# Optimization experiments

Hardware: AMD Instinct MI355X
Metric: run time of the kernel (lower is better)

## Reference

```python
import jax, jax.numpy as jnp
from jax import lax
import numpy as np

B, L, F = 4, 1024, 32
DM, NL, DS, DC, EX, NH = 256, 4, 16, 4, 2, 4
DI = EX * DM            # 512 inner channels
DTR = (DM + 15) // 16   # dt_rank = 16


def setup_inputs() -> dict:
    key = jax.random.key(0)
    ks = jax.random.split(key, 12)
    s = 0.02
    rn = lambda k, shape: jax.random.normal(k, shape, jnp.float32) * s
    return dict(
        x=jax.random.normal(ks[0], (B, L, F), jnp.float32),
        proj_w=rn(ks[1], (DM, F)), proj_b=jnp.zeros((DM,), jnp.float32),
        inproj_w=rn(ks[2], (NL, 2 * DI, DM)),
        conv_w=rn(ks[3], (NL, DI, DC)), conv_b=jnp.zeros((NL, DI), jnp.float32),
        xproj_w=rn(ks[4], (NL, DTR + 2 * DS, DI)),
        dtproj_w=rn(ks[5], (NL, DI, DTR)), dtproj_b=rn(ks[6], (NL, DI)),
        A_log=jnp.tile(jnp.log(jnp.arange(1, DS + 1, dtype=jnp.float32))[None, None, :], (NL, DI, 1)),
        Dp=jnp.ones((NL, DI), jnp.float32),
        outproj_w=rn(ks[7], (NL, DM, DI)),
        ln_g=jnp.ones((NL, DM), jnp.float32), ln_b=jnp.zeros((NL, DM), jnp.float32),
        head_w1=rn(ks[8], (DM, DM)), head_b1=jnp.zeros((DM,), jnp.float32),
        head_w2=rn(ks[9], (NH, DM)), head_b2=jnp.zeros((NH,), jnp.float32),
    )


def _layernorm(x, g, b, eps=1e-5):
    mu = x.mean(axis=-1, keepdims=True)
    var = ((x - mu) ** 2).mean(axis=-1, keepdims=True)
    return (x - mu) * lax.rsqrt(var + eps) * g + b


def _mamba(x, inw, cw, cb, xpw, dtw, dtb, A_log, Dp, outw):
    b, l, _ = x.shape
    xz = x @ inw.T                       # (b,l,2*DI)
    u, z = xz[..., :DI], xz[..., DI:]
    # causal depthwise conv1d, kernel DC
    up = jnp.pad(u, ((0, 0), (DC - 1, 0), (0, 0)))
    uc = sum(up[:, k:k + l, :] * cw[:, k] for k in range(DC)) + cb
    uc = jax.nn.silu(uc)
    dbc = uc @ xpw.T                     # (b,l,DTR+2*DS)
    dt, Bc, Cc = dbc[..., :DTR], dbc[..., DTR:DTR + DS], dbc[..., DTR + DS:]
    delta = jax.nn.softplus(dt @ dtw.T + dtb)   # (b,l,DI)
    A = -jnp.exp(A_log)                  # (DI,DS)

    def step(h, inp):
        d_t, B_t, C_t, u_t = inp         # (b,DI),(b,DS),(b,DS),(b,DI)
        h = jnp.exp(d_t[..., None] * A) * h + (d_t * u_t)[..., None] * B_t[:, None, :]
        return h, jnp.einsum('bdn,bn->bd', h, C_t)

    h0 = jnp.zeros((b, DI, DS), x.dtype)
    xs = tuple(jnp.swapaxes(a, 0, 1) for a in (delta, Bc, Cc, uc))
    _, ys = lax.scan(step, h0, xs)       # ys: (l,b,DI)
    y = jnp.swapaxes(ys, 0, 1) + uc * Dp
    return (y * jax.nn.silu(z)) @ outw.T


def reference(x, proj_w, proj_b, inproj_w, conv_w, conv_b, xproj_w, dtproj_w, dtproj_b,
              A_log, Dp, outproj_w, ln_g, ln_b, head_w1, head_b1, head_w2, head_b2):
    h = x @ proj_w.T + proj_b
    for i in range(NL):
        blk = _mamba(h, inproj_w[i], conv_w[i], conv_b[i], xproj_w[i],
                     dtproj_w[i], dtproj_b[i], A_log[i], Dp[i], outproj_w[i])
        h = h + _layernorm(blk, ln_g[i], ln_b[i])
    p = h.mean(axis=1)                   # (b,DM) pool over time
    hid = jax.nn.relu(p @ head_w1.T + head_b1)
    return hid @ head_w2.T + head_b2     # (b,NH)
```

## Files before the change

kernel.cpp:

```cpp
#include <hip/hip_runtime.h>
#include <hip/hip_fp16.h>
#include <math.h>

#define LTOT 1024
#define BB   4
#define F_IN 32
#define DM   256
#define DI   512
#define DS   16
#define DTRN 16
#define NXP  48
#define NLAY 4
#define NH   4
#define NC   16
#define CLEN 64
#define ROWS (BB*LTOT)

typedef _Float16 half8 __attribute__((ext_vector_type(8)));
typedef float f32x16 __attribute__((ext_vector_type(16)));

__device__ __forceinline__ float siluf_(float x) { return x / (1.0f + expf(-x)); }
__device__ __forceinline__ float softplusf_(float x) {
    if (x > 20.f) return x;
    if (x < -20.f) return expf(x);
    return log1pf(expf(x));
}

__device__ __forceinline__ void split16(float x, unsigned short& hi, unsigned short& lo) {
    __half h = __float2half(x);
    hi = *(unsigned short*)&h;
    float r = x - __half2float(h);
    __half l = __float2half(r);
    lo = *(unsigned short*)&l;
}

__device__ __forceinline__ size_t fragAddr(int r, int k, int Kd) {
    return ((size_t)((r >> 5) * (Kd >> 4) + (k >> 4)) << 9)
         + (size_t)(((((k >> 3) & 1) << 5) + (r & 31)) * 8 + (k & 7));
}

__global__ __launch_bounds__(256) void k_init(const float* __restrict__ x,
                                              const float* __restrict__ pw,
                                              const float* __restrict__ pb,
                                              const float* __restrict__ inw,
                                              const float* __restrict__ outw,
                                              float* __restrict__ h,
                                              unsigned short* __restrict__ hh,
                                              unsigned short* __restrict__ hl,
                                              unsigned short* __restrict__ iwh,
                                              unsigned short* __restrict__ iwl,
                                              unsigned short* __restrict__ owh,
                                              unsigned short* __restrict__ owl) {
    __shared__ float wl[DM][33];
    __shared__ float xl[16][32];
    int bid = blockIdx.x, t = threadIdx.x;
    if (bid < 1536) {
        int q = bid * 256 + t;
        ushort4 h4, l4;
        if (q < 262144) {
            float4 v = ((const float4*)inw)[q];
            split16(v.x, h4.x, l4.x); split16(v.y, h4.y, l4.y);
            split16(v.z, h4.z, l4.z); split16(v.w, h4.w, l4.w);
            int row = q >> 6, k0 = (q & 63) * 4;
            int lay = row >> 10, rIn = row & 1023;
            size_t fa = (size_t)lay * 262144 + fragAddr(rIn, k0, 256);
            *(ushort4*)(iwh + fa) = h4;
            *(ushort4*)(iwl + fa) = l4;
        } else {
            int rq = q - 262144;
            float4 v = ((const float4*)outw)[rq];
            split16(v.x, h4.x, l4.x); split16(v.y, h4.y, l4.y);
            split16(v.z, h4.z, l4.z); split16(v.w, h4.w, l4.w);
            int row = rq >> 7, k0 = (rq & 127) * 4;
            int lay = row >> 8, rIn = row & 255;
            size_t fa = (size_t)lay * 131072 + fragAddr(rIn, k0, 512);
            *(ushort4*)(owh + fa) = h4;
            *(ushort4*)(owl + fa) = l4;
        }
        return;
    }
    int r0 = (bid - 1536) * 16;
    for (int i = t; i < DM * 32 / 4; i += 256) {
        float4 v = ((const float4*)pw)[i];
        int c = i / 8, k = (i % 8) * 4;
        wl[c][k] = v.x; wl[c][k + 1] = v.y; wl[c][k + 2] = v.z; wl[c][k + 3] = v.w;
    }
    for (int i = t; i < 16 * 32 / 4; i += 256) {
        float4 v = ((const float4*)(x + (size_t)r0 * F_IN))[i];
        int r = i / 8, k = (i % 8) * 4;
        xl[r][k] = v.x; xl[r][k + 1] = v.y; xl[r][k + 2] = v.z; xl[r][k + 3] = v.w;
    }
    __syncthreads();
    int c = t;
    float bias = pb[c];
    float acc[16];
#pragma unroll
    for (int r = 0; r < 16; ++r) acc[r] = bias;
    for (int k = 0; k < 32; ++k) {
        float w = wl[c][k];
#pragma unroll
        for (int r = 0; r < 16; ++r) acc[r] = fmaf(xl[r][k], w, acc[r]);
    }
#pragma unroll
    for (int r = 0; r < 16; ++r) {
        int rr = r0 + r;
        h[(size_t)rr * DM + c] = acc[r];
        unsigned short vh, vl; split16(acc[r], vh, vl);
        size_t fa = fragAddr(rr, c, 256);
        hh[fa] = vh; hl[fa] = vl;
    }
}

__global__ __launch_bounds__(256) void k_gemm_xz(const unsigned short* __restrict__ Ahp,
                                                 const unsigned short* __restrict__ Alp,
                                                 const unsigned short* __restrict__ Bhp,
                                                 const unsigned short* __restrict__ Blp,
                                                 float* __restrict__ C) {
    int t = threadIdx.x;
    int bx = blockIdx.x & 7;
    int by = blockIdx.x >> 3;
    int lane = t & 63, wid = t >> 6;
    int fr = lane & 31, fg = lane >> 5;
    int wr = wid >> 1, wc = wid & 1;
    int rt = by * 2 + wr;
    int ct0 = bx * 4 + wc * 2;
    const half8* pAh = (const half8*)Ahp + (size_t)rt * 1024 + lane;
    const half8* pAl = (const half8*)Alp + (size_t)rt * 1024 + lane;
    const half8* pB0h = (const half8*)Bhp + (size_t)ct0 * 1024 + lane;
    const half8* pB0l = (const half8*)Blp + (size_t)ct0 * 1024 + lane;
    const half8* pB1h = pB0h + 1024;
    const half8* pB1l = pB0l + 1024;
    f32x16 acc[2] = {};
    half8 ah = pAh[0], al = pAl[0];
    half8 b0h = pB0h[0], b0l = pB0l[0], b1h = pB1h[0], b1l = pB1l[0];
#pragma unroll
    for (int kt = 0; kt < 16; ++kt) {
        half8 nah, nal, nb0h, nb0l, nb1h, nb1l;
        if (kt < 15) {
            int o = (kt + 1) * 64;
            nah = pAh[o]; nal = pAl[o];
            nb0h = pB0h[o]; nb0l = pB0l[o];
            nb1h = pB1h[o]; nb1l = pB1l[o];
        }
        acc[0] = __builtin_amdgcn_mfma_f32_32x32x16_f16(ah, b0h, acc[0], 0, 0, 0);
        acc[0] = __builtin_amdgcn_mfma_f32_32x32x16_f16(ah, b0l, acc[0], 0, 0, 0);
        acc[0] = __builtin_amdgcn_mfma_f32_32x32x16_f16(al, b0h, acc[0], 0, 0, 0);
        acc[1] = __builtin_amdgcn_mfma_f32_32x32x16_f16(ah, b1h, acc[1], 0, 0, 0);
        acc[1] = __builtin_amdgcn_mfma_f32_32x32x16_f16(ah, b1l, acc[1], 0, 0, 0);
        acc[1] = __builtin_amdgcn_mfma_f32_32x32x16_f16(al, b1h, acc[1], 0, 0, 0);
        if (kt < 15) { ah = nah; al = nal; b0h = nb0h; b0l = nb0l; b1h = nb1h; b1l = nb1l; }
    }
    float* Cp = C + (size_t)(by * 64 + wr * 32) * 1024 + bx * 128 + wc * 64;
#pragma unroll
    for (int fc = 0; fc < 2; ++fc) {
#pragma unroll
        for (int reg = 0; reg < 16; ++reg) {
            int row = (reg & 3) + 8 * (reg >> 2) + 4 * fg;
            Cp[(size_t)row * 1024 + fc * 32 + fr] = acc[fc][reg];
        }
    }
}

__global__ __launch_bounds__(256) void k_dbcp(const float* __restrict__ xz,
                                              const float* __restrict__ cw,
                                              const float* __restrict__ cb,
                                              const float* __restrict__ xpw,
                                              float* __restrict__ uc,
                                              float* __restrict__ dbp) {
    __shared__ float us[32][132];
    __shared__ float wsd[48][132];
    int t = threadIdx.x;
    int kp = blockIdx.x & 3;
    int r0 = (blockIdx.x >> 2) * 32;
    int k0 = kp * 128;
    float4* us4 = (float4*)us;
    float4* ws4 = (float4*)wsd;
#pragma unroll
    for (int j = 0; j < 4; ++j) {
        int i = t + j * 256;
        int r = i >> 5, kq = i & 31;
        int rr = r0 + r, d = k0 + kq * 4;
        int tt = rr & (LTOT - 1);
        float4 acc = make_float4(cb[d], cb[d + 1], cb[d + 2], cb[d + 3]);
#pragma unroll
        for (int k = 0; k < 4; ++k) {
            int ts = tt - 3 + k;
            if (ts < 0) continue;
            float4 u = *(const float4*)(xz + (size_t)(rr - 3 + k) * 1024 + d);
            acc.x = fmaf(u.x, cw[(d + 0) * 4 + k], acc.x);
            acc.y = fmaf(u.y, cw[(d + 1) * 4 + k], acc.y);
            acc.z = fmaf(u.z, cw[(d + 2) * 4 + k], acc.z);
            acc.w = fmaf(u.w, cw[(d + 3) * 4 + k], acc.w);
        }
        acc.x = siluf_(acc.x); acc.y = siluf_(acc.y); acc.z = siluf_(acc.z); acc.w = siluf_(acc.w);
        us4[r * 33 + kq] = acc;
        *(float4*)(uc + (size_t)rr * DI + d) = acc;
    }
#pragma unroll
    for (int j = 0; j < 6; ++j) {
        int i = t + j * 256;
        int r = i >> 5, kq = i & 31;
        ws4[r * 33 + kq] = *(const float4*)(xpw + (size_t)r * DI + k0 + kq * 4);
    }
    __syncthreads();
    int tx = t & 15, ty = t >> 4;
    const float4* ua = us4 + (ty * 2) * 33;
    const float4* ub = ua + 33;
    const float4* w0p = ws4 + (tx * 3) * 33;
    const float4* w1p = w0p + 33;
    const float4* w2p = w0p + 66;
    float acc[2][3] = {};
#pragma unroll 4
    for (int kq = 0; kq < 32; ++kq) {
        float4 u0 = ua[kq], u1 = ub[kq];
        float4 w0 = w0p[kq], w1 = w1p[kq], w2 = w2p[kq];
        acc[0][0] = fmaf(u0.x, w0.x, acc[0][0]); acc[0][0] = fmaf(u0.y, w0.y, acc[0][0]);
        acc[0][0] = fmaf(u0.z, w0.z, acc[0][0]); acc[0][0] = fmaf(u0.w, w0.w, acc[0][0]);
        acc[0][1] = fmaf(u0.x, w1.x, acc[0][1]); acc[0][1] = fmaf(u0.y, w1.y, acc[0][1]);
        acc[0][1] = fmaf(u0.z, w1.z, acc[0][1]); acc[0][1] = fmaf(u0.w, w1.w, acc[0][1]);
        acc[0][2] = fmaf(u0.x, w2.x, acc[0][2]); acc[0][2] = fmaf(u0.y, w2.y, acc[0][2]);
        acc[0][2] = fmaf(u0.z, w2.z, acc[0][2]); acc[0][2] = fmaf(u0.w, w2.w, acc[0][2]);
        acc[1][0] = fmaf(u1.x, w0.x, acc[1][0]); acc[1][0] = fmaf(u1.y, w0.y, acc[1][0]);
        acc[1][0] = fmaf(u1.z, w0.z, acc[1][0]); acc[1][0] = fmaf(u1.w, w0.w, acc[1][0]);
        acc[1][1] = fmaf(u1.x, w1.x, acc[1][1]); acc[1][1] = fmaf(u1.y, w1.y, acc[1][1]);
        acc[1][1] = fmaf(u1.z, w1.z, acc[1][1]); acc[1][1] = fmaf(u1.w, w1.w, acc[1][1]);
        acc[1][2] = fmaf(u1.x, w2.x, acc[1][2]); acc[1][2] = fmaf(u1.y, w2.y, acc[1][2]);
        acc[1][2] = fmaf(u1.z, w2.z, acc[1][2]); acc[1][2] = fmaf(u1.w, w2.w, acc[1][2]);
    }
    float* outp = dbp + (size_t)(r0 + ty * 2) * 192 + kp * 48 + tx * 3;
    outp[0] = acc[0][0]; outp[1] = acc[0][1]; outp[2] = acc[0][2];
    outp[192] = acc[1][0]; outp[193] = acc[1][1]; outp[194] = acc[1][2];
}

__global__ __launch_bounds__(256) void k_dbcr(const float* __restrict__ dbp,
                                              const float* __restrict__ dtw,
                                              const float* __restrict__ dtb,
                                              float* __restrict__ delta,
                                              float* __restrict__ BC) {
    __shared__ float dbl[16][NXP];
    int t = threadIdx.x;
    int r0 = blockIdx.x * 16;
    {
        int r = t >> 4, c3 = (t & 15) * 3;
        const float* pp = dbp + (size_t)(r0 + r) * 192 + c3;
#pragma unroll
        for (int j = 0; j < 3; ++j) {
            float s = pp[j] + pp[48 + j] + pp[96 + j] + pp[144 + j];
            dbl[r][c3 + j] = s;
            int cj = c3 + j;
            if (cj >= 16) BC[(size_t)(r0 + r) * 32 + (cj - 16)] = s;
        }
    }
    __syncthreads();
    {
        int c0 = t * 2;
        float wd0[16], wd1[16];
        const float4* q0 = (const float4*)(dtw + (size_t)c0 * 16);
        const float4* q1 = (const float4*)(dtw + (size_t)(c0 + 1) * 16);
#pragma unroll
        for (int j = 0; j < 4; ++j) { *(float4*)&wd0[j * 4] = q0[j]; *(float4*)&wd1[j * 4] = q1[j]; }
        float bb0 = dtb[c0], bb1 = dtb[c0 + 1];
        for (int r = 0; r < 16; ++r) {
            float s0 = bb0, s1 = bb1;
#pragma unroll
            for (int k = 0; k < 16; ++k) {
                float dv = dbl[r][k];
                s0 = fmaf(dv, wd0[k], s0);
                s1 = fmaf(dv, wd1[k], s1);
            }
            *(float2*)(delta + (size_t)(r0 + r) * DI + c0) =
                make_float2(softplusf_(s0), softplusf_(s1));
        }
    }
}

__global__ __launch_bounds__(256) void k_scanA(const float* __restrict__ delta,
                                               const float* __restrict__ uc,
                                               const float* __restrict__ BC,
                                               const float* __restrict__ A_log,
                                               float* __restrict__ P,
                                               float* __restrict__ hL) {
    __shared__ float2 du2[CLEN][16];
    __shared__ float  Bl[CLEN][16];
    int bid = blockIdx.x;
    int c = bid & 15, dblk = (bid >> 4) & 31, b = bid >> 9;
    int d0 = dblk * 16, t0 = c * CLEN;
    int t = threadIdx.x;
    {
        int row = t >> 2, hf = (t & 3) * 4;
        size_t rbase = (size_t)(b * LTOT + t0 + row);
        float4 dv = *(const float4*)(delta + rbase * DI + d0 + hf);
        float4 uv = *(const float4*)(uc + rbase * DI + d0 + hf);
        float4* dst = (float4*)&du2[row][hf];
        dst[0] = make_float4(dv.x, uv.x, dv.y, uv.y);
        dst[1] = make_float4(dv.z, uv.z, dv.w, uv.w);
        *(float4*)&Bl[row][hf] = *(const float4*)(BC + rbase * 32 + hf);
    }
    __syncthreads();
    int n = t & 15, dn = t >> 4;
    float Ac = -expf(A_log[(size_t)(d0 + dn) * DS + n]);
    float h = 0.f, Pp = 1.f;
#pragma unroll 8
    for (int k = 0; k < CLEN; ++k) {
        float2 du = du2[k][dn];
        float Bv = Bl[k][n];
        float a = expf(du.x * Ac);
        Pp *= a;
        h = fmaf(a, h, du.x * du.y * Bv);
    }
    size_t idx = ((size_t)(b * NC + c)) * (DI * DS) + (size_t)d0 * DS + t;
    P[idx] = Pp;
    hL[idx] = h;
}

__global__ __launch_bounds__(256) void k_scanC(const float* __restrict__ delta,
                                               const float* __restrict__ uc,
                                               const float* __restrict__ BC,
                                               const float* __restrict__ A_log,
                                               const float* __restrict__ P,
                                               const float* __restrict__ hL,
                                               const float* __restrict__ Dp,
                                               const float* __restrict__ xz,
                                               unsigned short* __restrict__ yh,
                                               unsigned short* __restrict__ yl) {
    __shared__ float2 du2[CLEN][16];
    __shared__ float2 bc2[CLEN][16];
    __shared__ float  ytmp[16][16][20];
    int bid = blockIdx.x;
    int c = bid & 15, dblk = (bid >> 4) & 31, b = bid >> 9;
    int d0 = dblk * 16, t0 = c * CLEN;
    int t = threadIdx.x;
    {
        int row = t >> 2, hf = (t & 3) * 4;
        size_t rbase = (size_t)(b * LTOT + t0 + row);
        float4 dv = *(const float4*)(delta + rbase * DI + d0 + hf);
        float4 uv = *(const float4*)(uc + rbase * DI + d0 + hf);
        float4* dst = (float4*)&du2[row][hf];
        dst[0] = make_float4(dv.x, uv.x, dv.y, uv.y);
        dst[1] = make_float4(dv.z, uv.z, dv.w, uv.w);
        float4 bv = *(const float4*)(BC + rbase * 32 + hf);
        float4 cv = *(const float4*)(BC + rbase * 32 + 16 + hf);
        float4* bdst = (float4*)&bc2[row][hf];
        bdst[0] = make_float4(bv.x, cv.x, bv.y, cv.y);
        bdst[1] = make_float4(bv.z, cv.z, bv.w, cv.w);
    }
    __syncthreads();
    int n = t & 15, dn = t >> 4;
    float Ac = -expf(A_log[(size_t)(d0 + dn) * DS + n]);
    float Hin = 0.f;
    for (int cc = 0; cc < c; ++cc) {
        size_t idx = ((size_t)(b * NC + cc)) * (DI * DS) + (size_t)d0 * DS + t;
        Hin = fmaf(P[idx], Hin, hL[idx]);
    }
    float h = Hin;
    int rdn = t & 15, rk = t >> 4;
    float DpV = Dp[d0 + rdn];
    for (int s = 0; s < CLEN / 16; ++s) {
#pragma unroll
        for (int kk = 0; kk < 16; ++kk) {
            int k = s * 16 + kk;
            float2 du = du2[k][dn];
            float2 bc = bc2[k][n];
            float a = expf(du.x * Ac);
            h = fmaf(a, h, du.x * du.y * bc.x);
            ytmp[kk][dn][n] = h * bc.y;
        }
        __syncthreads();
        {
            const float* rowp = &ytmp[rk][rdn][0];
            float4 v0 = *(const float4*)(rowp + 0);
            float4 v1 = *(const float4*)(rowp + 4);
            float4 v2 = *(const float4*)(rowp + 8);
            float4 v3 = *(const float4*)(rowp + 12);
            float y = ((v0.x + v0.y) + (v0.z + v0.w)) + ((v1.x + v1.y) + (v1.z + v1.w))
                    + ((v2.x + v2.y) + (v2.z + v2.w)) + ((v3.x + v3.y) + (v3.z + v3.w));
            float uu = du2[s * 16 + rk][rdn].y;
            size_t rb2 = (size_t)(b * LTOT + t0 + s * 16 + rk);
            float z = xz[rb2 * 1024 + 512 + d0 + rdn];
            float val = fmaf(uu, DpV, y) * siluf_(z);
            unsigned short vh, vl; split16(val, vh, vl);
            size_t fa = fragAddr((int)rb2, d0 + rdn, 512);
            yh[fa] = vh; yl[fa] = vl;
        }
        __syncthreads();
    }
}

__global__ __launch_bounds__(256) void k_gemm_out(const unsigned short* __restrict__ Ahp,
                                                  const unsigned short* __restrict__ Alp,
                                                  const unsigned short* __restrict__ Bhp,
                                                  const unsigned short* __restrict__ Blp,
                                                  float* __restrict__ p01,
                                                  float* __restrict__ p23) {
    int t = threadIdx.x;
    int bx = blockIdx.x & 1;
    int by = (blockIdx.x >> 1) & 63;
    int kp = blockIdx.x >> 7;
    int lane = t & 63, wid = t >> 6;
    int fr = lane & 31, fg = lane >> 5;
    int wr = wid >> 1, wc = wid & 1;
    int rt = by * 2 + wr;
    int ct0 = bx * 4 + wc * 2;
    const half8* pAh = (const half8*)Ahp + (size_t)rt * 2048 + (size_t)kp * 512 + lane;
    const half8* pAl = (const half8*)Alp + (size_t)rt * 2048 + (size_t)kp * 512 + lane;
    const half8* pB0h = (const half8*)Bhp + (size_t)ct0 * 2048 + (size_t)kp * 512 + lane;
    const half8* pB0l = (const half8*)Blp + (size_t)ct0 * 2048 + (size_t)kp * 512 + lane;
    const half8* pB1h = pB0h + 2048;
    const half8* pB1l = pB0l + 2048;
    f32x16 acc[2] = {};
    half8 ah = pAh[0], al = pAl[0];
    half8 b0h = pB0h[0], b0l = pB0l[0], b1h = pB1h[0], b1l = pB1l[0];
#pragma unroll
    for (int kt = 0; kt < 8; ++kt) {
        half8 nah, nal, nb0h, nb0l, nb1h, nb1l;
        if (kt < 7) {
            int o = (kt + 1) * 64;
            nah = pAh[o]; nal = pAl[o];
            nb0h = pB0h[o]; nb0l = pB0l[o];
            nb1h = pB1h[o]; nb1l = pB1l[o];
        }
        acc[0] = __builtin_amdgcn_mfma_f32_32x32x16_f16(ah, b0h, acc[0], 0, 0, 0);
        acc[0] = __builtin_amdgcn_mfma_f32_32x32x16_f16(ah, b0l, acc[0], 0, 0, 0);
        acc[0] = __builtin_amdgcn_mfma_f32_32x32x16_f16(al, b0h, acc[0], 0, 0, 0);
        acc[1] = __builtin_amdgcn_mfma_f32_32x32x16_f16(ah, b1h, acc[1], 0, 0, 0);
        acc[1] = __builtin_amdgcn_mfma_f32_32x32x16_f16(ah, b1l, acc[1], 0, 0, 0);
        acc[1] = __builtin_amdgcn_mfma_f32_32x32x16_f16(al, b1h, acc[1], 0, 0, 0);
        if (kt < 7) { ah = nah; al = nal; b0h = nb0h; b0l = nb0l; b1h = nb1h; b1l = nb1l; }
    }
    float* pbase = (kp < 2 ? p01 : p23) + (size_t)(kp & 1) * (ROWS * DM);
    float* Cp = pbase + (size_t)(by * 64 + wr * 32) * DM + bx * 128 + wc * 64;
#pragma unroll
    for (int fc = 0; fc < 2; ++fc) {
#pragma unroll
        for (int reg = 0; reg < 16; ++reg) {
            int row = (reg & 3) + 8 * (reg >> 2) + 4 * fg;
            Cp[(size_t)row * DM + fc * 32 + fr] = acc[fc][reg];
        }
    }
}

__global__ __launch_bounds__(256) void k_ln_res(const float* __restrict__ p01,
                                                const float* __restrict__ p23,
                                                const float* __restrict__ g,
                                                const float* __restrict__ bb,
                                                float* __restrict__ h,
                                                unsigned short* __restrict__ hh,
                                                unsigned short* __restrict__ hl) {
    __shared__ float scratch[4];
    int r = blockIdx.x, t = threadIdx.x;
    size_t idx = (size_t)r * DM + t;
    float v = p01[idx] + p01[idx + (size_t)ROWS * DM] + p23[idx] + p23[idx + (size_t)ROWS * DM];
    float s = v;
#pragma unroll
    for (int m = 32; m >= 1; m >>= 1) s += __shfl_xor(s, m, 64);
    if ((t & 63) == 0) scratch[t >> 6] = s;
    __syncthreads();
    float mu = (scratch[0] + scratch[1] + scratch[2] + scratch[3]) * (1.f / DM);
    __syncthreads();
    float d = v - mu;
    float s2 = d * d;
#pragma unroll
    for (int m = 32; m >= 1; m >>= 1) s2 += __shfl_xor(s2, m, 64);
    if ((t & 63) == 0) scratch[t >> 6] = s2;
    __syncthreads();
    float var = (scratch[0] + scratch[1] + scratch[2] + scratch[3]) * (1.f / DM);
    float rstd = 1.f / sqrtf(var + 1e-5f);
    float nv = h[idx] + d * rstd * g[t] + bb[t];
    h[idx] = nv;
    unsigned short vh, vl; split16(nv, vh, vl);
    size_t fa = fragAddr(r, t, 256);
    hh[fa] = vh; hl[fa] = vl;
}

__global__ __launch_bounds__(256) void k_meanp(const float* __restrict__ h,
                                               float* __restrict__ part) {
    int bid = blockIdx.x;
    int b = bid >> 3, g = bid & 7;
    int t = threadIdx.x;
    float s = 0.f;
    for (int k = 0; k < 128; ++k)
        s += h[(size_t)(b * LTOT + g * 128 + k) * DM + t];
    part[(size_t)bid * DM + t] = s;
}

__global__ __launch_bounds__(256) void k_head(const float* __restrict__ part,
                                              const float* __restrict__ w1,
                                              const float* __restrict__ b1,
                                              const float* __restrict__ w2,
                                              const float* __restrict__ b2,
                                              float* __restrict__ out) {
    __shared__ float pl[DM], hl[DM];
    int b = blockIdx.x, t = threadIdx.x;
    float s = 0.f;
    for (int g = 0; g < 8; ++g) s += part[(size_t)(b * 8 + g) * DM + t];
    pl[t] = s * (1.f / LTOT);
    __syncthreads();
    float a = b1[t];
    for (int k = 0; k < DM; ++k) a = fmaf(pl[k], w1[(size_t)t * DM + k], a);
    hl[t] = fmaxf(a, 0.f);
    __syncthreads();
    if (t < NH) {
        float o = b2[t];
        for (int k = 0; k < DM; ++k) o = fmaf(hl[k], w2[(size_t)t * DM + k], o);
        out[b * NH + t] = o;
    }
}

extern "C" void kernel_launch(void* const* d_in, const int* in_sizes, int n_in,
                              void* d_out, int out_size, void* d_ws, size_t ws_size,
                              hipStream_t stream) {
    const float* x        = (const float*)d_in[0];
    const float* proj_w   = (const float*)d_in[1];
    const float* proj_b   = (const float*)d_in[2];
    const float* inproj_w = (const float*)d_in[3];
    const float* conv_w   = (const float*)d_in[4];
    const float* conv_b   = (const float*)d_in[5];
    const float* xproj_w  = (const float*)d_in[6];
    const float* dtproj_w = (const float*)d_in[7];
    const float* dtproj_b = (const float*)d_in[8];
    const float* A_log    = (const float*)d_in[9];
    const float* Dp       = (const float*)d_in[10];
    const float* outproj_w= (const float*)d_in[11];
    const float* ln_g     = (const float*)d_in[12];
    const float* ln_b     = (const float*)d_in[13];
    const float* head_w1  = (const float*)d_in[14];
    const float* head_b1  = (const float*)d_in[15];
    const float* head_w2  = (const float*)d_in[16];
    const float* head_b2  = (const float*)d_in[17];

    float* ws    = (float*)d_ws;
    float* h     = ws;
    float* xz    = h + 1048576;
    float* uc    = xz + 4194304;
    float* dbp   = uc + 2097152;
    float* delta = dbp + 786432;
    float* BC    = delta + 2097152;
    float* Pbuf  = BC + 131072;
    float* hLbuf = Pbuf + 524288;
    float* p01   = hLbuf + 524288;
    float* p23   = p01 + 2097152;
    float* part  = p23 + 2097152;
    unsigned short* h_hi  = (unsigned short*)(part + 8192);
    unsigned short* h_lo  = h_hi + 1048576;
    unsigned short* y_hi  = h_lo + 1048576;
    unsigned short* y_lo  = y_hi + 2097152;
    unsigned short* iw_hi = y_lo + 2097152;
    unsigned short* iw_lo = iw_hi + 1048576;
    unsigned short* ow_hi = iw_lo + 1048576;
    unsigned short* ow_lo = ow_hi + 524288;

    k_init<<<1792, 256, 0, stream>>>(x, proj_w, proj_b, inproj_w, outproj_w,
                                     h, h_hi, h_lo, iw_hi, iw_lo, ow_hi, ow_lo);

    for (int i = 0; i < NLAY; ++i) {
        const float* cwi  = conv_w + (size_t)i * DI * 4;
        const float* cbi  = conv_b + (size_t)i * DI;
        const float* xpw  = xproj_w + (size_t)i * NXP * DI;
        const float* dtw  = dtproj_w + (size_t)i * DI * DTRN;
        const float* dtb  = dtproj_b + (size_t)i * DI;
        const float* Ali  = A_log + (size_t)i * DI * DS;
        const float* Dpi  = Dp + (size_t)i * DI;
        const float* gi   = ln_g + (size_t)i * DM;
        const float* bi   = ln_b + (size_t)i * DM;

        k_gemm_xz<<<512, 256, 0, stream>>>(h_hi, h_lo,
                                           iw_hi + (size_t)i * 262144, iw_lo + (size_t)i * 262144, xz);
        k_dbcp<<<512, 256, 0, stream>>>(xz, cwi, cbi, xpw, uc, dbp);
        k_dbcr<<<ROWS / 16, 256, 0, stream>>>(dbp, dtw, dtb, delta, BC);
        k_scanA<<<BB * 32 * NC, 256, 0, stream>>>(delta, uc, BC, Ali, Pbuf, hLbuf);
        k_scanC<<<BB * 32 * NC, 256, 0, stream>>>(delta, uc, BC, Ali, Pbuf, hLbuf, Dpi, xz, y_hi, y_lo);
        k_gemm_out<<<512, 256, 0, stream>>>(y_hi, y_lo,
                                            ow_hi + (size_t)i * 131072, ow_lo + (size_t)i * 131072,
                                            p01, p23);
        k_ln_res<<<ROWS, 256, 0, stream>>>(p01, p23, gi, bi, h, h_hi, h_lo);
    }

    k_meanp<<<32, 256, 0, stream>>>(h, part);
    k_head<<<BB, 256, 0, stream>>>(part, head_w1, head_b1, head_w2, head_b2, (float*)d_out);
}
```

Measured before the change: 484.4 us.

## Fuse x_proj partial and reduce kernels; batch layernorm rows per block

Merges the split-K x_proj kernel and its reduction/dt_proj kernel into one kernel. Each block now covers 16 rows and loops over all four K chunks, keeping the partial sums in registers, so the dbp intermediate buffer and one launch per layer go away. Separately, the layernorm-residual kernel now processes 8 rows per block instead of one, which reuses the gamma/beta loads across rows. The cost is fewer blocks (256 and 512) with more serial work and extra barriers per block, which lowers parallelism.

```diff
diff --git a/kernel.cpp b/kernel.cpp
--- a/kernel.cpp
+++ b/kernel.cpp
@@ -161,95 +161,86 @@
     }
 }
 
-__global__ __launch_bounds__(256) void k_dbcp(const float* __restrict__ xz,
-                                              const float* __restrict__ cw,
-                                              const float* __restrict__ cb,
-                                              const float* __restrict__ xpw,
-                                              float* __restrict__ uc,
-                                              float* __restrict__ dbp) {
-    __shared__ float us[32][132];
-    __shared__ float wsd[48][132];
-    int t = threadIdx.x;
-    int kp = blockIdx.x & 3;
-    int r0 = (blockIdx.x >> 2) * 32;
-    int k0 = kp * 128;
-    float4* us4 = (float4*)us;
-    float4* ws4 = (float4*)wsd;
-#pragma unroll
-    for (int j = 0; j < 4; ++j) {
-        int i = t + j * 256;
-        int r = i >> 5, kq = i & 31;
-        int rr = r0 + r, d = k0 + kq * 4;
-        int tt = rr & (LTOT - 1);
-        float4 acc = make_float4(cb[d], cb[d + 1], cb[d + 2], cb[d + 3]);
-#pragma unroll
-        for (int k = 0; k < 4; ++k) {
-            int ts = tt - 3 + k;
-            if (ts < 0) continue;
-            float4 u = *(const float4*)(xz + (size_t)(rr - 3 + k) * 1024 + d);
-            acc.x = fmaf(u.x, cw[(d + 0) * 4 + k], acc.x);
-            acc.y = fmaf(u.y, cw[(d + 1) * 4 + k], acc.y);
-            acc.z = fmaf(u.z, cw[(d + 2) * 4 + k], acc.z);
-            acc.w = fmaf(u.w, cw[(d + 3) * 4 + k], acc.w);
-        }
-        acc.x = siluf_(acc.x); acc.y = siluf_(acc.y); acc.z = siluf_(acc.z); acc.w = siluf_(acc.w);
-        us4[r * 33 + kq] = acc;
-        *(float4*)(uc + (size_t)rr * DI + d) = acc;
-    }
-#pragma unroll
-    for (int j = 0; j < 6; ++j) {
-        int i = t + j * 256;
-        int r = i >> 5, kq = i & 31;
-        ws4[r * 33 + kq] = *(const float4*)(xpw + (size_t)r * DI + k0 + kq * 4);
-    }
-    __syncthreads();
-    int tx = t & 15, ty = t >> 4;
-    const float4* ua = us4 + (ty * 2) * 33;
-    const float4* ub = ua + 33;
-    const float4* w0p = ws4 + (tx * 3) * 33;
-    const float4* w1p = w0p + 33;
-    const float4* w2p = w0p + 66;
-    float acc[2][3] = {};
+__global__ __launch_bounds__(256) void k_dbc(const float* __restrict__ xz,
+                                             const float* __restrict__ cw,
+                                             const float* __restrict__ cb,
+                                             const float* __restrict__ xpw,
+                                             const float* __restrict__ dtw,
+                                             const float* __restrict__ dtb,
+                                             float* __restrict__ uc,
+                                             float* __restrict__ delta,
+                                             float* __restrict__ BC) {
+    __shared__ float4 us4[16 * 33];
+    __shared__ float4 ws4[48 * 33];
+    __shared__ float  dbl[16][NXP];
+    int t = threadIdx.x;
+    int r0 = blockIdx.x * 16;
+    int row = t >> 4, tx = t & 15;
+    float ps0[4], ps1[4], ps2[4];
+#pragma unroll
+    for (int kp = 0; kp < 4; ++kp) {
+        int k0 = kp * 128;
+#pragma unroll
+        for (int j = 0; j < 2; ++j) {
+            int i = t + j * 256;
+            int r = i >> 5, kq = i & 31;
+            int rr = r0 + r, d = k0 + kq * 4;
+            int tt = rr & (LTOT - 1);
+            float4 acc = make_float4(cb[d], cb[d + 1], cb[d + 2], cb[d + 3]);
+#pragma unroll
+            for (int k = 0; k < 4; ++k) {
+                int ts = tt - 3 + k;
+                if (ts < 0) continue;
+                float4 u = *(const float4*)(xz + (size_t)(rr - 3 + k) * 1024 + d);
+                acc.x = fmaf(u.x, cw[(d + 0) * 4 + k], acc.x);
+                acc.y = fmaf(u.y, cw[(d + 1) * 4 + k], acc.y);
+                acc.z = fmaf(u.z, cw[(d + 2) * 4 + k], acc.z);
+                acc.w = fmaf(u.w, cw[(d + 3) * 4 + k], acc.w);
+            }
+            acc.x = siluf_(acc.x); acc.y = siluf_(acc.y);
+            acc.z = siluf_(acc.z); acc.w = siluf_(acc.w);
+            us4[r * 33 + kq] = acc;
+            *(float4*)(uc + (size_t)rr * DI + d) = acc;
+        }
+#pragma unroll
+        for (int j = 0; j < 6; ++j) {
+            int i = t + j * 256;
+            int r = i >> 5, kq = i & 31;
+            ws4[r * 33 + kq] = *(const float4*)(xpw + (size_t)r * DI + k0 + kq * 4);
+        }
+        __syncthreads();
+        {
+            const float4* ua = us4 + row * 33;
+            const float4* w0p = ws4 + (tx * 3) * 33;
+            const float4* w1p = w0p + 33;
+            const float4* w2p = w0p + 66;
+            float a0 = 0.f, a1 = 0.f, a2 = 0.f;
 #pragma unroll 4
-    for (int kq = 0; kq < 32; ++kq) {
-        float4 u0 = ua[kq], u1 = ub[kq];
-        float4 w0 = w0p[kq], w1 = w1p[kq], w2 = w2p[kq];
-        acc[0][0] = fmaf(u0.x, w0.x, acc[0][0]); acc[0][0] = fmaf(u0.y, w0.y, acc[0][0]);
-        acc[0][0] = fmaf(u0.z, w0.z, acc[0][0]); acc[0][0] = fmaf(u0.w, w0.w, acc[0][0]);
-        acc[0][1] = fmaf(u0.x, w1.x, acc[0][1]); acc[0][1] = fmaf(u0.y, w1.y, acc[0][1]);
-        acc[0][1] = fmaf(u0.z, w1.z, acc[0][1]); acc[0][1] = fmaf(u0.w, w1.w, acc[0][1]);
-        acc[0][2] = fmaf(u0.x, w2.x, acc[0][2]); acc[0][2] = fmaf(u0.y, w2.y, acc[0][2]);
-        acc[0][2] = fmaf(u0.z, w2.z, acc[0][2]); acc[0][2] = fmaf(u0.w, w2.w, acc[0][2]);
-        acc[1][0] = fmaf(u1.x, w0.x, acc[1][0]); acc[1][0] = fmaf(u1.y, w0.y, acc[1][0]);
-        acc[1][0] = fmaf(u1.z, w0.z, acc[1][0]); acc[1][0] = fmaf(u1.w, w0.w, acc[1][0]);
-        acc[1][1] = fmaf(u1.x, w1.x, acc[1][1]); acc[1][1] = fmaf(u1.y, w1.y, acc[1][1]);
-        acc[1][1] = fmaf(u1.z, w1.z, acc[1][1]); acc[1][1] = fmaf(u1.w, w1.w, acc[1][1]);
-        acc[1][2] = fmaf(u1.x, w2.x, acc[1][2]); acc[1][2] = fmaf(u1.y, w2.y, acc[1][2]);
-        acc[1][2] = fmaf(u1.z, w2.z, acc[1][2]); acc[1][2] = fmaf(u1.w, w2.w, acc[1][2]);
-    }
-    float* outp = dbp + (size_t)(r0 + ty * 2) * 192 + kp * 48 + tx * 3;
-    outp[0] = acc[0][0]; outp[1] = acc[0][1]; outp[2] = acc[0][2];
-    outp[192] = acc[1][0]; outp[193] = acc[1][1]; outp[194] = acc[1][2];
-}
-
-__global__ __launch_bounds__(256) void k_dbcr(const float* __restrict__ dbp,
-                                              const float* __restrict__ dtw,
-                                              const float* __restrict__ dtb,
-                                              float* __restrict__ delta,
-                                              float* __restrict__ BC) {
-    __shared__ float dbl[16][NXP];
-    int t = threadIdx.x;
-    int r0 = blockIdx.x * 16;
+            for (int kq = 0; kq < 32; ++kq) {
+                float4 u0 = ua[kq];
+                float4 w0 = w0p[kq], w1 = w1p[kq], w2 = w2p[kq];
+                a0 = fmaf(u0.x, w0.x, a0); a0 = fmaf(u0.y, w0.y, a0);
+                a0 = fmaf(u0.z, w0.z, a0); a0 = fmaf(u0.w, w0.w, a0);
+                a1 = fmaf(u0.x, w1.x, a1); a1 = fmaf(u0.y, w1.y, a1);
+                a1 = fmaf(u0.z, w1.z, a1); a1 = fmaf(u0.w, w1.w, a1);
+                a2 = fmaf(u0.x, w2.x, a2); a2 = fmaf(u0.y, w2.y, a2);
+                a2 = fmaf(u0.z, w2.z, a2); a2 = fmaf(u0.w, w2.w, a2);
+            }
+            ps0[kp] = a0; ps1[kp] = a1; ps2[kp] = a2;
+        }
+        __syncthreads();
+    }
     {
-        int r = t >> 4, c3 = (t & 15) * 3;
-        const float* pp = dbp + (size_t)(r0 + r) * 192 + c3;
-#pragma unroll
-        for (int j = 0; j < 3; ++j) {
-            float s = pp[j] + pp[48 + j] + pp[96 + j] + pp[144 + j];
-            dbl[r][c3 + j] = s;
-            int cj = c3 + j;
-            if (cj >= 16) BC[(size_t)(r0 + r) * 32 + (cj - 16)] = s;
-        }
+        float s0 = ((ps0[0] + ps0[1]) + ps0[2]) + ps0[3];
+        float s1 = ((ps1[0] + ps1[1]) + ps1[2]) + ps1[3];
+        float s2 = ((ps2[0] + ps2[1]) + ps2[2]) + ps2[3];
+        int c3 = tx * 3;
+        dbl[row][c3 + 0] = s0;
+        dbl[row][c3 + 1] = s1;
+        dbl[row][c3 + 2] = s2;
+        if (c3 + 0 >= 16) BC[(size_t)(r0 + row) * 32 + (c3 + 0 - 16)] = s0;
+        if (c3 + 1 >= 16) BC[(size_t)(r0 + row) * 32 + (c3 + 1 - 16)] = s1;
+        if (c3 + 2 >= 16) BC[(size_t)(r0 + row) * 32 + (c3 + 2 - 16)] = s2;
     }
     __syncthreads();
     {
@@ -447,29 +438,35 @@
                                                 unsigned short* __restrict__ hh,
                                                 unsigned short* __restrict__ hl) {
     __shared__ float scratch[4];
-    int r = blockIdx.x, t = threadIdx.x;
-    size_t idx = (size_t)r * DM + t;
-    float v = p01[idx] + p01[idx + (size_t)ROWS * DM] + p23[idx] + p23[idx + (size_t)ROWS * DM];
-    float s = v;
-#pragma unroll
-    for (int m = 32; m >= 1; m >>= 1) s += __shfl_xor(s, m, 64);
-    if ((t & 63) == 0) scratch[t >> 6] = s;
-    __syncthreads();
-    float mu = (scratch[0] + scratch[1] + scratch[2] + scratch[3]) * (1.f / DM);
-    __syncthreads();
-    float d = v - mu;
-    float s2 = d * d;
-#pragma unroll
-    for (int m = 32; m >= 1; m >>= 1) s2 += __shfl_xor(s2, m, 64);
-    if ((t & 63) == 0) scratch[t >> 6] = s2;
-    __syncthreads();
-    float var = (scratch[0] + scratch[1] + scratch[2] + scratch[3]) * (1.f / DM);
-    float rstd = 1.f / sqrtf(var + 1e-5f);
-    float nv = h[idx] + d * rstd * g[t] + bb[t];
-    h[idx] = nv;
-    unsigned short vh, vl; split16(nv, vh, vl);
-    size_t fa = fragAddr(r, t, 256);
-    hh[fa] = vh; hl[fa] = vl;
+    int t = threadIdx.x;
+    int r0 = blockIdx.x * 8;
+    float gv = g[t], bv = bb[t];
+    for (int rr = 0; rr < 8; ++rr) {
+        int r = r0 + rr;
+        size_t idx = (size_t)r * DM + t;
+        float v = p01[idx] + p01[idx + (size_t)ROWS * DM] + p23[idx] + p23[idx + (size_t)ROWS * DM];
+        float s = v;
+#pragma unroll
+        for (int m = 32; m >= 1; m >>= 1) s += __shfl_xor(s, m, 64);
+        if ((t & 63) == 0) scratch[t >> 6] = s;
+        __syncthreads();
+        float mu = (scratch[0] + scratch[1] + scratch[2] + scratch[3]) * (1.f / DM);
+        __syncthreads();
+        float d = v - mu;
+        float s2 = d * d;
+#pragma unroll
+        for (int m = 32; m >= 1; m >>= 1) s2 += __shfl_xor(s2, m, 64);
+        if ((t & 63) == 0) scratch[t >> 6] = s2;
+        __syncthreads();
+        float var = (scratch[0] + scratch[1] + scratch[2] + scratch[3]) * (1.f / DM);
+        float rstd = 1.f / sqrtf(var + 1e-5f);
+        float nv = h[idx] + d * rstd * gv + bv;
+        h[idx] = nv;
+        unsigned short vh, vl; split16(nv, vh, vl);
+        size_t fa = fragAddr(r, t, 256);
+        hh[fa] = vh; hl[fa] = vl;
+        __syncthreads();
+    }
 }
 
 __global__ __launch_bounds__(256) void k_meanp(const float* __restrict__ h,
@@ -532,8 +529,7 @@
     float* h     = ws;
     float* xz    = h + 1048576;
     float* uc    = xz + 4194304;
-    float* dbp   = uc + 2097152;
-    float* delta = dbp + 786432;
+    float* delta = uc + 2097152;
     float* BC    = delta + 2097152;
     float* Pbuf  = BC + 131072;
     float* hLbuf = Pbuf + 524288;
@@ -565,14 +561,13 @@
 
         k_gemm_xz<<<512, 256, 0, stream>>>(h_hi, h_lo,
                                            iw_hi + (size_t)i * 262144, iw_lo + (size_t)i * 262144, xz);
-        k_dbcp<<<512, 256, 0, stream>>>(xz, cwi, cbi, xpw, uc, dbp);
-        k_dbcr<<<ROWS / 16, 256, 0, stream>>>(dbp, dtw, dtb, delta, BC);
+        k_dbc<<<256, 256, 0, stream>>>(xz, cwi, cbi, xpw, dtw, dtb, uc, delta, BC);
         k_scanA<<<BB * 32 * NC, 256, 0, stream>>>(delta, uc, BC, Ali, Pbuf, hLbuf);
         k_scanC<<<BB * 32 * NC, 256, 0, stream>>>(delta, uc, BC, Ali, Pbuf, hLbuf, Dpi, xz, y_hi, y_lo);
         k_gemm_out<<<512, 256, 0, stream>>>(y_hi, y_lo,
                                             ow_hi + (size_t)i * 131072, ow_lo + (size_t)i * 131072,
                                             p01, p23);
-        k_ln_res<<<ROWS, 256, 0, stream>>>(p01, p23, gi, bi, h, h_hi, h_lo);
+        k_ln_res<<<512, 256, 0, stream>>>(p01, p23, gi, bi, h, h_hi, h_lo);
     }
 
     k_meanp<<<32, 256, 0, stream>>>(h, part);
```

Measured after the change: 518.8 us. +7.1%, slower.

## Replace chunked two-pass selective scan with single-pass sequential scan; batch LN rows

Applied to the files above, without the earlier changes.

Drops the two-kernel chunked scan, which computed per-chunk decay products and end states and then rebuilt each chunk's incoming state from a serial prefix. In its place is one kernel where each block walks all 16 chunks of a (batch, 16-channel) slice in order, carrying the state in a register. This removes the P/hL workspace traffic, one launch per layer and the redundant first pass. The cost is parallelism: only 128 blocks run long serial loops, and each chunk's global loads are not overlapped with compute. Separately, the layernorm-residual kernel now handles 8 rows per block to cut block count and per-block overhead.

```diff
diff --git a/kernel.cpp b/kernel.cpp
--- a/kernel.cpp
+++ b/kernel.cpp
@@ -274,115 +274,72 @@
     }
 }
 
-__global__ __launch_bounds__(256) void k_scanA(const float* __restrict__ delta,
-                                               const float* __restrict__ uc,
-                                               const float* __restrict__ BC,
-                                               const float* __restrict__ A_log,
-                                               float* __restrict__ P,
-                                               float* __restrict__ hL) {
-    __shared__ float2 du2[CLEN][16];
-    __shared__ float  Bl[CLEN][16];
-    int bid = blockIdx.x;
-    int c = bid & 15, dblk = (bid >> 4) & 31, b = bid >> 9;
-    int d0 = dblk * 16, t0 = c * CLEN;
-    int t = threadIdx.x;
-    {
-        int row = t >> 2, hf = (t & 3) * 4;
-        size_t rbase = (size_t)(b * LTOT + t0 + row);
-        float4 dv = *(const float4*)(delta + rbase * DI + d0 + hf);
-        float4 uv = *(const float4*)(uc + rbase * DI + d0 + hf);
-        float4* dst = (float4*)&du2[row][hf];
-        dst[0] = make_float4(dv.x, uv.x, dv.y, uv.y);
-        dst[1] = make_float4(dv.z, uv.z, dv.w, uv.w);
-        *(float4*)&Bl[row][hf] = *(const float4*)(BC + rbase * 32 + hf);
-    }
-    __syncthreads();
-    int n = t & 15, dn = t >> 4;
-    float Ac = -expf(A_log[(size_t)(d0 + dn) * DS + n]);
-    float h = 0.f, Pp = 1.f;
-#pragma unroll 8
-    for (int k = 0; k < CLEN; ++k) {
-        float2 du = du2[k][dn];
-        float Bv = Bl[k][n];
-        float a = expf(du.x * Ac);
-        Pp *= a;
-        h = fmaf(a, h, du.x * du.y * Bv);
-    }
-    size_t idx = ((size_t)(b * NC + c)) * (DI * DS) + (size_t)d0 * DS + t;
-    P[idx] = Pp;
-    hL[idx] = h;
-}
-
-__global__ __launch_bounds__(256) void k_scanC(const float* __restrict__ delta,
-                                               const float* __restrict__ uc,
-                                               const float* __restrict__ BC,
-                                               const float* __restrict__ A_log,
-                                               const float* __restrict__ P,
-                                               const float* __restrict__ hL,
-                                               const float* __restrict__ Dp,
-                                               const float* __restrict__ xz,
-                                               unsigned short* __restrict__ yh,
-                                               unsigned short* __restrict__ yl) {
+__global__ __launch_bounds__(256) void k_scan(const float* __restrict__ delta,
+                                              const float* __restrict__ uc,
+                                              const float* __restrict__ BC,
+                                              const float* __restrict__ A_log,
+                                              const float* __restrict__ Dp,
+                                              const float* __restrict__ xz,
+                                              unsigned short* __restrict__ yh,
+                                              unsigned short* __restrict__ yl) {
     __shared__ float2 du2[CLEN][16];
     __shared__ float2 bc2[CLEN][16];
     __shared__ float  ytmp[16][16][20];
     int bid = blockIdx.x;
-    int c = bid & 15, dblk = (bid >> 4) & 31, b = bid >> 9;
-    int d0 = dblk * 16, t0 = c * CLEN;
-    int t = threadIdx.x;
-    {
-        int row = t >> 2, hf = (t & 3) * 4;
-        size_t rbase = (size_t)(b * LTOT + t0 + row);
-        float4 dv = *(const float4*)(delta + rbase * DI + d0 + hf);
-        float4 uv = *(const float4*)(uc + rbase * DI + d0 + hf);
-        float4* dst = (float4*)&du2[row][hf];
-        dst[0] = make_float4(dv.x, uv.x, dv.y, uv.y);
-        dst[1] = make_float4(dv.z, uv.z, dv.w, uv.w);
-        float4 bv = *(const float4*)(BC + rbase * 32 + hf);
-        float4 cv = *(const float4*)(BC + rbase * 32 + 16 + hf);
-        float4* bdst = (float4*)&bc2[row][hf];
-        bdst[0] = make_float4(bv.x, cv.x, bv.y, cv.y);
-        bdst[1] = make_float4(bv.z, cv.z, bv.w, cv.w);
-    }
-    __syncthreads();
+    int dblk = bid & 31, b = bid >> 5;
+    int d0 = dblk * 16;
+    int t = threadIdx.x;
+    int row = t >> 2, hf = (t & 3) * 4;
     int n = t & 15, dn = t >> 4;
+    int rdn = t & 15, rk = t >> 4;
     float Ac = -expf(A_log[(size_t)(d0 + dn) * DS + n]);
-    float Hin = 0.f;
-    for (int cc = 0; cc < c; ++cc) {
-        size_t idx = ((size_t)(b * NC + cc)) * (DI * DS) + (size_t)d0 * DS + t;
-        Hin = fmaf(P[idx], Hin, hL[idx]);
-    }
-    float h = Hin;
-    int rdn = t & 15, rk = t >> 4;
     float DpV = Dp[d0 + rdn];
-    for (int s = 0; s < CLEN / 16; ++s) {
-#pragma unroll
-        for (int kk = 0; kk < 16; ++kk) {
-            int k = s * 16 + kk;
-            float2 du = du2[k][dn];
-            float2 bc = bc2[k][n];
-            float a = expf(du.x * Ac);
-            h = fmaf(a, h, du.x * du.y * bc.x);
-            ytmp[kk][dn][n] = h * bc.y;
+    float h = 0.f;
+    for (int c = 0; c < NC; ++c) {
+        int t0 = c * CLEN;
+        {
+            size_t rbase = (size_t)(b * LTOT + t0 + row);
+            float4 dv = *(const float4*)(delta + rbase * DI + d0 + hf);
+            float4 uv = *(const float4*)(uc + rbase * DI + d0 + hf);
+            float4* dst = (float4*)&du2[row][hf];
+            dst[0] = make_float4(dv.x, uv.x, dv.y, uv.y);
+            dst[1] = make_float4(dv.z, uv.z, dv.w, uv.w);
+            float4 bv = *(const float4*)(BC + rbase * 32 + hf);
+            float4 cv = *(const float4*)(BC + rbase * 32 + 16 + hf);
+            float4* bdst = (float4*)&bc2[row][hf];
+            bdst[0] = make_float4(bv.x, cv.x, bv.y, cv.y);
+            bdst[1] = make_float4(bv.z, cv.z, bv.w, cv.w);
         }
         __syncthreads();
-        {
-            const float* rowp = &ytmp[rk][rdn][0];
-            float4 v0 = *(const float4*)(rowp + 0);
-            float4 v1 = *(const float4*)(rowp + 4);
-            float4 v2 = *(const float4*)(rowp + 8);
-            float4 v3 = *(const float4*)(rowp + 12);
-            float y = ((v0.x + v0.y) + (v0.z + v0.w)) + ((v1.x + v1.y) + (v1.z + v1.w))
-                    + ((v2.x + v2.y) + (v2.z + v2.w)) + ((v3.x + v3.y) + (v3.z + v3.w));
-            float uu = du2[s * 16 + rk][rdn].y;
-            size_t rb2 = (size_t)(b * LTOT + t0 + s * 16 + rk);
-            float z = xz[rb2 * 1024 + 512 + d0 + rdn];
-            float val = fmaf(uu, DpV, y) * siluf_(z);
-            unsigned short vh, vl; split16(val, vh, vl);
-            size_t fa = fragAddr((int)rb2, d0 + rdn, 512);
-            yh[fa] = vh; yl[fa] = vl;
-        }
-        __syncthreads();
+        for (int s = 0; s < CLEN / 16; ++s) {
+#pragma unroll
+            for (int kk = 0; kk < 16; ++kk) {
+                int k = s * 16 + kk;
+                float2 du = du2[k][dn];
+                float2 bc = bc2[k][n];
+                float a = expf(du.x * Ac);
+                h = fmaf(a, h, du.x * du.y * bc.x);
+                ytmp[kk][dn][n] = h * bc.y;
+            }
+            __syncthreads();
+            {
+                const float* rowp = &ytmp[rk][rdn][0];
+                float4 v0 = *(const float4*)(rowp + 0);
+                float4 v1 = *(const float4*)(rowp + 4);
+                float4 v2 = *(const float4*)(rowp + 8);
+                float4 v3 = *(const float4*)(rowp + 12);
+                float y = ((v0.x + v0.y) + (v0.z + v0.w)) + ((v1.x + v1.y) + (v1.z + v1.w))
+                        + ((v2.x + v2.y) + (v2.z + v2.w)) + ((v3.x + v3.y) + (v3.z + v3.w));
+                float uu = du2[s * 16 + rk][rdn].y;
+                size_t rb2 = (size_t)(b * LTOT + t0 + s * 16 + rk);
+                float z = xz[rb2 * 1024 + 512 + d0 + rdn];
+                float val = fmaf(uu, DpV, y) * siluf_(z);
+                unsigned short vh, vl; split16(val, vh, vl);
+                size_t fa = fragAddr((int)rb2, d0 + rdn, 512);
+                yh[fa] = vh; yl[fa] = vl;
+            }
+            __syncthreads();
+        }
     }
 }
 
@@ -447,29 +404,35 @@
                                                 unsigned short* __restrict__ hh,
                                                 unsigned short* __restrict__ hl) {
     __shared__ float scratch[4];
-    int r = blockIdx.x, t = threadIdx.x;
-    size_t idx = (size_t)r * DM + t;
-    float v = p01[idx] + p01[idx + (size_t)ROWS * DM] + p23[idx] + p23[idx + (size_t)ROWS * DM];
-    float s = v;
-#pragma unroll
-    for (int m = 32; m >= 1; m >>= 1) s += __shfl_xor(s, m, 64);
-    if ((t & 63) == 0) scratch[t >> 6] = s;
-    __syncthreads();
-    float mu = (scratch[0] + scratch[1] + scratch[2] + scratch[3]) * (1.f / DM);
-    __syncthreads();
-    float d = v - mu;
-    float s2 = d * d;
-#pragma unroll
-    for (int m = 32; m >= 1; m >>= 1) s2 += __shfl_xor(s2, m, 64);
-    if ((t & 63) == 0) scratch[t >> 6] = s2;
-    __syncthreads();
-    float var = (scratch[0] + scratch[1] + scratch[2] + scratch[3]) * (1.f / DM);
-    float rstd = 1.f / sqrtf(var + 1e-5f);
-    float nv = h[idx] + d * rstd * g[t] + bb[t];
-    h[idx] = nv;
-    unsigned short vh, vl; split16(nv, vh, vl);
-    size_t fa = fragAddr(r, t, 256);
-    hh[fa] = vh; hl[fa] = vl;
+    int t = threadIdx.x;
+    int r0 = blockIdx.x * 8;
+    float gv = g[t], bv = bb[t];
+    for (int rr = 0; rr < 8; ++rr) {
+        int r = r0 + rr;
+        size_t idx = (size_t)r * DM + t;
+        float v = p01[idx] + p01[idx + (size_t)ROWS * DM] + p23[idx] + p23[idx + (size_t)ROWS * DM];
+        float s = v;
+#pragma unroll
+        for (int m = 32; m >= 1; m >>= 1) s += __shfl_xor(s, m, 64);
+        if ((t & 63) == 0) scratch[t >> 6] = s;
+        __syncthreads();
+        float mu = (scratch[0] + scratch[1] + scratch[2] + scratch[3]) * (1.f / DM);
+        __syncthreads();
+        float d = v - mu;
+        float s2 = d * d;
+#pragma unroll
+        for (int m = 32; m >= 1; m >>= 1) s2 += __shfl_xor(s2, m, 64);
+        if ((t & 63) == 0) scratch[t >> 6] = s2;
+        __syncthreads();
+        float var = (scratch[0] + scratch[1] + scratch[2] + scratch[3]) * (1.f / DM);
+        float rstd = 1.f / sqrtf(var + 1e-5f);
+        float nv = h[idx] + d * rstd * gv + bv;
+        h[idx] = nv;
+        unsigned short vh, vl; split16(nv, vh, vl);
+        size_t fa = fragAddr(r, t, 256);
+        hh[fa] = vh; hl[fa] = vl;
+        __syncthreads();
+    }
 }
 
 __global__ __launch_bounds__(256) void k_meanp(const float* __restrict__ h,
@@ -535,9 +498,7 @@
     float* dbp   = uc + 2097152;
     float* delta = dbp + 786432;
     float* BC    = delta + 2097152;
-    float* Pbuf  = BC + 131072;
-    float* hLbuf = Pbuf + 524288;
-    float* p01   = hLbuf + 524288;
+    float* p01   = BC + 131072;
     float* p23   = p01 + 2097152;
     float* part  = p23 + 2097152;
     unsigned short* h_hi  = (unsigned short*)(part + 8192);
@@ -567,12 +528,11 @@
                                            iw_hi + (size_t)i * 262144, iw_lo + (size_t)i * 262144, xz);
         k_dbcp<<<512, 256, 0, stream>>>(xz, cwi, cbi, xpw, uc, dbp);
         k_dbcr<<<ROWS / 16, 256, 0, stream>>>(dbp, dtw, dtb, delta, BC);
-        k_scanA<<<BB * 32 * NC, 256, 0, stream>>>(delta, uc, BC, Ali, Pbuf, hLbuf);
-        k_scanC<<<BB * 32 * NC, 256, 0, stream>>>(delta, uc, BC, Ali, Pbuf, hLbuf, Dpi, xz, y_hi, y_lo);
+        k_scan<<<BB * 32, 256, 0, stream>>>(delta, uc, BC, Ali, Dpi, xz, y_hi, y_lo);
         k_gemm_out<<<512, 256, 0, stream>>>(y_hi, y_lo,
                                             ow_hi + (size_t)i * 131072, ow_lo + (size_t)i * 131072,
                                             p01, p23);
-        k_ln_res<<<ROWS, 256, 0, stream>>>(p01, p23, gi, bi, h, h_hi, h_lo);
+        k_ln_res<<<512, 256, 0, stream>>>(p01, p23, gi, bi, h, h_hi, h_lo);
     }
 
     k_meanp<<<32, 256, 0, stream>>>(h, part);
```

Result: slower. 774.6 us (+59.9%).
